# Performance work log

Hardware: AMD Instinct MI355X
Metric: run time of the kernel (lower is better)

The kernel has to match this reference:

```python
import jax, jax.numpy as jnp
import numpy as np

B, N, C, H, DEPTH, MLP = 8, 1024, 768, 12, 8, 3072
HD = C // H
SCALE = HD ** -0.5
EPS = 1e-5


def layer_norm(x, g, b):
    mu = jnp.mean(x, -1, keepdims=True)
    var = jnp.mean((x - mu) ** 2, -1, keepdims=True)
    return (x - mu) / jnp.sqrt(var + EPS) * g + b


def setup_inputs() -> dict:
    key = jax.random.key(0)
    ks = jax.random.split(key, 8)
    s = 0.02
    return {
        "x": jax.random.normal(ks[0], (B, N, C), jnp.float32),
        "ln1_g": jnp.ones((DEPTH, C), jnp.float32),
        "ln1_b": jnp.zeros((DEPTH, C), jnp.float32),
        "wqkv": jax.random.normal(ks[1], (DEPTH, C, 3 * C), jnp.float32) * s,
        "wproj": jax.random.normal(ks[2], (DEPTH, C, C), jnp.float32) * s,
        "bproj": jnp.zeros((DEPTH, C), jnp.float32),
        "ln2_g": jnp.ones((DEPTH, C), jnp.float32),
        "ln2_b": jnp.zeros((DEPTH, C), jnp.float32),
        "w1": jax.random.normal(ks[3], (DEPTH, C, MLP), jnp.float32) * s,
        "b1": jnp.zeros((DEPTH, MLP), jnp.float32),
        "w2": jax.random.normal(ks[4], (DEPTH, MLP, C), jnp.float32) * s,
        "b2": jnp.zeros((DEPTH, C), jnp.float32),
    }


def reference(x, ln1_g, ln1_b, wqkv, wproj, bproj, ln2_g, ln2_b, w1, b1, w2, b2):
    def body(h, p):
        g1, be1, wq, wp, bp, g2, be2, wf1, bf1, wf2, bf2 = p
        # --- attention block: Residual(PreNorm(SelfAttention)) ---
        y = layer_norm(h, g1, be1)
        qkv = (y @ wq).reshape(B, N, 3, H, HD)
        qkv = jnp.transpose(qkv, (2, 0, 3, 1, 4))  # [3, B, H, N, HD]
        q, k, v = qkv[0], qkv[1], qkv[2]
        logits = jnp.einsum("bhnd,bhmd->bhnm", q, k) * SCALE
        # source applies softmax twice (faithful to original)
        attn = jax.nn.softmax(jax.nn.softmax(logits, axis=-1), axis=-1)
        o = jnp.einsum("bhnm,bhmd->bhnd", attn, v)
        o = jnp.transpose(o, (0, 2, 1, 3)).reshape(B, N, C)
        h = h + o @ wp + bp
        # --- FFN block: Residual(PreNorm(FeedForward)) ---
        y2 = layer_norm(h, g2, be2)
        f = jax.nn.relu(y2 @ wf1 + bf1) @ wf2 + bf2
        return h + f, None

    out, _ = jax.lax.scan(body, x, (ln1_g, ln1_b, wqkv, wproj, bproj, ln2_g, ln2_b, w1, b1, w2, b2))
    return out
```

## Files before the change

kernel.cpp:

```cpp
#include <hip/hip_runtime.h>

#define DEPTHL 8
#define BZ 8
#define SEQ 1024
#define CDIM 768
#define HEADS 12
#define HDIM 64
#define MLPD 3072
#define TOK (BZ*SEQ)
#define QKVN (3*CDIM)

typedef __attribute__((ext_vector_type(8))) short vshort8;
typedef __attribute__((ext_vector_type(4))) short vshort4;
typedef __attribute__((ext_vector_type(4))) float vfloat4;

__device__ __forceinline__ short bf16_bits(float f) {
  union { float f; unsigned u; } x; x.f = f;
  unsigned r = (x.u + 0x7FFFu + ((x.u >> 16) & 1u)) >> 16;
  return (short)r;
}

#define GL16(g, l) __builtin_amdgcn_global_load_lds( \
    (const __attribute__((address_space(1))) unsigned int*)(g), \
    (__attribute__((address_space(3))) unsigned int*)(l), 16, 0, 0)

__global__ __launch_bounds__(256) void wconv_t(const float* __restrict__ in,
                                               short* __restrict__ out,
                                               int K, int N) {
  __shared__ float tile[32][33];
  const long d = blockIdx.z;
  in  += d * (long)K * N;
  out += d * (long)N * K;
  const int n0 = blockIdx.x * 32, k0 = blockIdx.y * 32;
  const int tx = threadIdx.x & 31, ty = threadIdx.x >> 5;
#pragma unroll
  for (int i = 0; i < 4; i++)
    tile[ty + 8*i][tx] = in[(long)(k0 + ty + 8*i) * N + n0 + tx];
  __syncthreads();
#pragma unroll
  for (int i = 0; i < 4; i++)
    out[(long)(n0 + ty + 8*i) * K + k0 + tx] = bf16_bits(tile[tx][ty + 8*i]);
}

__global__ __launch_bounds__(256) void vtrans(const short* __restrict__ qkv,
                                              short* __restrict__ vt) {
  __shared__ short tile[32][34];
  const int bh = blockIdx.z;
  const int b = bh / HEADS, hh = bh % HEADS;
  const int t0 = blockIdx.x * 32, d0 = blockIdx.y * 32;
  const int tx = threadIdx.x & 31, ty = threadIdx.x >> 5;
  const short* src = qkv + ((long)b * SEQ + t0) * QKVN + 2 * CDIM + hh * HDIM + d0;
#pragma unroll
  for (int i = 0; i < 4; i++)
    tile[ty + 8*i][tx] = src[(long)(ty + 8*i) * QKVN + tx];
  __syncthreads();
  short* dst = vt + (long)bh * HDIM * SEQ + (long)d0 * SEQ + t0;
#pragma unroll
  for (int i = 0; i < 4; i++)
    dst[(long)(ty + 8*i) * SEQ + tx] = tile[tx][ty + 8*i];
}

__global__ __launch_bounds__(192) void ln_fwd(const float* __restrict__ h,
                                              const float* __restrict__ g,
                                              const float* __restrict__ be,
                                              short* __restrict__ y) {
  __shared__ float red[3];
  const int row = blockIdx.x;
  const int tid = threadIdx.x;
  const float4 v = ((const float4*)(h + (long)row * CDIM))[tid];
  float s = v.x + v.y + v.z + v.w;
#pragma unroll
  for (int m = 32; m >= 1; m >>= 1) s += __shfl_xor(s, m);
  if ((tid & 63) == 0) red[tid >> 6] = s;
  __syncthreads();
  const float mu = (red[0] + red[1] + red[2]) * (1.0f / CDIM);
  float dx = v.x - mu, dy = v.y - mu, dz = v.z - mu, dw = v.w - mu;
  float q = dx*dx + dy*dy + dz*dz + dw*dw;
  __syncthreads();
#pragma unroll
  for (int m = 32; m >= 1; m >>= 1) q += __shfl_xor(q, m);
  if ((tid & 63) == 0) red[tid >> 6] = q;
  __syncthreads();
  const float rstd = rsqrtf((red[0] + red[1] + red[2]) * (1.0f / CDIM) + 1e-5f);
  const float4 g4 = ((const float4*)g)[tid];
  const float4 b4 = ((const float4*)be)[tid];
  vshort4 o;
  o[0] = bf16_bits(dx * rstd * g4.x + b4.x);
  o[1] = bf16_bits(dy * rstd * g4.y + b4.y);
  o[2] = bf16_bits(dz * rstd * g4.z + b4.z);
  o[3] = bf16_bits(dw * rstd * g4.w + b4.w);
  *(vshort4*)(y + (long)row * CDIM + tid * 4) = o;
}

template<int EPI>
__global__ __launch_bounds__(256) void gemm_bt(const short* __restrict__ A,
                                               const short* __restrict__ Bt,
                                               const float* __restrict__ bias,
                                               void* __restrict__ Cout,
                                               int M, int N, int K) {
  __shared__ short As[128 * 32];
  __shared__ short Bs[128 * 32];
  const int tid = threadIdx.x;
  const int wid = tid >> 6, lane = tid & 63;
  const int lg = lane >> 4, lr = lane & 15;
  const int wm = wid >> 1, wn = wid & 1;
  const long by = blockIdx.y;
  const long bx = blockIdx.x;

  vfloat4 acc[4][4];
#pragma unroll
  for (int i = 0; i < 4; i++)
#pragma unroll
    for (int j = 0; j < 4; j++) acc[i][j] = (vfloat4){0.f, 0.f, 0.f, 0.f};

  const int c = wid * 64 + lane;
  const short* Ag0 = A  + (by * 128 +      (c >> 2)) * (long)K + (c & 3) * 8;
  const short* Ag1 = A  + (by * 128 + 64 + (c >> 2)) * (long)K + (c & 3) * 8;
  const short* Bg0 = Bt + (bx * 128 +      (c >> 2)) * (long)K + (c & 3) * 8;
  const short* Bg1 = Bt + (bx * 128 + 64 + (c >> 2)) * (long)K + (c & 3) * 8;
  short* Al = As + c * 8;
  short* Bl = Bs + c * 8;

  for (int kk = 0; kk < K; kk += 32) {
    __syncthreads();
    GL16(Ag0 + kk, Al);
    GL16(Ag1 + kk, Al + 2048);
    GL16(Bg0 + kk, Bl);
    GL16(Bg1 + kk, Bl + 2048);
    __syncthreads();
    vshort8 a[4], b[4];
#pragma unroll
    for (int mt = 0; mt < 4; mt++)
      a[mt] = *(const vshort8*)(As + (wm * 64 + mt * 16 + lr) * 32 + lg * 8);
#pragma unroll
    for (int nt = 0; nt < 4; nt++)
      b[nt] = *(const vshort8*)(Bs + (wn * 64 + nt * 16 + lr) * 32 + lg * 8);
#pragma unroll
    for (int mt = 0; mt < 4; mt++)
#pragma unroll
      for (int nt = 0; nt < 4; nt++)
        acc[mt][nt] = __builtin_amdgcn_mfma_f32_16x16x32_bf16(a[mt], b[nt], acc[mt][nt], 0, 0, 0);
  }

  const long row0 = by * 128 + wm * 64;
  const long col0 = bx * 128 + wn * 64;
#pragma unroll
  for (int mt = 0; mt < 4; mt++) {
#pragma unroll
    for (int nt = 0; nt < 4; nt++) {
      const long col = col0 + nt * 16 + lr;
      float bv = 0.f;
      if (EPI != 0) bv = bias[col];
#pragma unroll
      for (int r = 0; r < 4; r++) {
        const long row = row0 + mt * 16 + lg * 4 + r;
        float v = acc[mt][nt][r];
        if (EPI == 0) {
          ((short*)Cout)[row * N + col] = bf16_bits(v);
        } else if (EPI == 1) {
          v += bv; v = v > 0.f ? v : 0.f;
          ((short*)Cout)[row * N + col] = bf16_bits(v);
        } else {
          float* hp = (float*)Cout + row * N + col;
          *hp = *hp + v + bv;
        }
      }
    }
  }
}

__global__ __launch_bounds__(256) void attn_fused2(const short* __restrict__ qkv,
                                                   const short* __restrict__ vt,
                                                   short* __restrict__ o) {
  __shared__ short P_lds[16 * 1024];
  __shared__ float redm[4][16], redz[4][16], redt[4][16];
  const int qt = blockIdx.x, bh = blockIdx.y;
  const int b = bh / HEADS, hh = bh % HEADS;
  const int tid = threadIdx.x, wid = tid >> 6, lane = tid & 63;
  const int lg = lane >> 4, lr = lane & 15;
  const long tokbase = (long)b * SEQ;
  const short* qbase = qkv + tokbase * QKVN + hh * HDIM;
  const short* kbase = qbase + CDIM;
  const short* vtb = vt + (long)bh * HDIM * SEQ;

  vshort8 qf[2];
#pragma unroll
  for (int ks = 0; ks < 2; ks++)
    qf[ks] = *(const vshort8*)(qbase + (long)(qt * 16 + lr) * QKVN + ks * 32 + lg * 8);

  vfloat4 s[16];
#pragma unroll
  for (int i = 0; i < 16; i++) {
    const int n0 = wid * 256 + i * 16;
    vfloat4 acc = (vfloat4){0.f, 0.f, 0.f, 0.f};
#pragma unroll
    for (int ks = 0; ks < 2; ks++) {
      vshort8 kf = *(const vshort8*)(kbase + (long)(n0 + lr) * QKVN + ks * 32 + lg * 8);
      acc = __builtin_amdgcn_mfma_f32_16x16x32_bf16(kf, qf[ks], acc, 0, 0, 0);
    }
    s[i][0] = acc[0] * 0.125f; s[i][1] = acc[1] * 0.125f;
    s[i][2] = acc[2] * 0.125f; s[i][3] = acc[3] * 0.125f;
  }

  vfloat4 mv = s[0];
#pragma unroll
  for (int i = 1; i < 16; i++) {
    mv[0] = fmaxf(mv[0], s[i][0]); mv[1] = fmaxf(mv[1], s[i][1]);
    mv[2] = fmaxf(mv[2], s[i][2]); mv[3] = fmaxf(mv[3], s[i][3]);
  }
  float m = fmaxf(fmaxf(mv[0], mv[1]), fmaxf(mv[2], mv[3]));
  m = fmaxf(m, __shfl_xor(m, 16));
  m = fmaxf(m, __shfl_xor(m, 32));
  if (lane < 16) redm[wid][lr] = m;
  __syncthreads();
  m = fmaxf(fmaxf(redm[0][lr], redm[1][lr]), fmaxf(redm[2][lr], redm[3][lr]));

  float z = 0.f;
#pragma unroll
  for (int i = 0; i < 16; i++) {
#pragma unroll
    for (int r = 0; r < 4; r++) { s[i][r] = __expf(s[i][r] - m); z += s[i][r]; }
  }
  z += __shfl_xor(z, 16);
  z += __shfl_xor(z, 32);
  if (lane < 16) redz[wid][lr] = z;
  __syncthreads();
  z = redz[0][lr] + redz[1][lr] + redz[2][lr] + redz[3][lr];
  const float rz = 1.0f / z;

  float t2 = 0.f;
#pragma unroll
  for (int i = 0; i < 16; i++) {
#pragma unroll
    for (int r = 0; r < 4; r++) { s[i][r] = __expf(s[i][r] * rz); t2 += s[i][r]; }
  }
  t2 += __shfl_xor(t2, 16);
  t2 += __shfl_xor(t2, 32);
  if (lane < 16) redt[wid][lr] = t2;
  __syncthreads();
  t2 = redt[0][lr] + redt[1][lr] + redt[2][lr] + redt[3][lr];
  const float rt = 1.0f / t2;

#pragma unroll
  for (int i = 0; i < 16; i++) {
    const int sbase = lr * 1024 + wid * 256 + i * 16 + lg * 4;
    const int byt = (sbase * 2) ^ ((lr & 7) << 4);
    vshort4 pk;
    pk[0] = bf16_bits(s[i][0] * rt); pk[1] = bf16_bits(s[i][1] * rt);
    pk[2] = bf16_bits(s[i][2] * rt); pk[3] = bf16_bits(s[i][3] * rt);
    *(vshort4*)((char*)P_lds + byt) = pk;
  }
  __syncthreads();

  const int dt = wid;
  vfloat4 oacc = (vfloat4){0.f, 0.f, 0.f, 0.f};
  const short* vrow = vtb + (long)(dt * 16 + lr) * SEQ + lg * 8;
#pragma unroll 8
  for (int win = 0; win < 32; win++) {
    const int abyt = (lr * 2048 + win * 64 + lg * 16) ^ ((lr & 7) << 4);
    vshort8 af = *(const vshort8*)((char*)P_lds + abyt);
    vshort8 bfr = *(const vshort8*)(vrow + win * 32);
    oacc = __builtin_amdgcn_mfma_f32_16x16x32_bf16(af, bfr, oacc, 0, 0, 0);
  }

#pragma unroll
  for (int r = 0; r < 4; r++) {
    const long row = tokbase + qt * 16 + lg * 4 + r;
    o[row * CDIM + hh * HDIM + dt * 16 + lr] = bf16_bits(oacc[r]);
  }
}

extern "C" void kernel_launch(void* const* d_in, const int* in_sizes, int n_in,
                              void* d_out, int out_size, void* d_ws, size_t ws_size,
                              hipStream_t stream) {
  const float* x     = (const float*)d_in[0];
  const float* ln1_g = (const float*)d_in[1];
  const float* ln1_b = (const float*)d_in[2];
  const float* wqkv  = (const float*)d_in[3];
  const float* wproj = (const float*)d_in[4];
  const float* bproj = (const float*)d_in[5];
  const float* ln2_g = (const float*)d_in[6];
  const float* ln2_b = (const float*)d_in[7];
  const float* w1    = (const float*)d_in[8];
  const float* b1    = (const float*)d_in[9];
  const float* w2    = (const float*)d_in[10];
  const float* b2    = (const float*)d_in[11];
  float* h = (float*)d_out;

  char* ws = (char*)d_ws;
  short* wqkv_t  = (short*)ws; ws += (size_t)DEPTHL * QKVN * CDIM * 2;
  short* wproj_t = (short*)ws; ws += (size_t)DEPTHL * CDIM * CDIM * 2;
  short* w1_t    = (short*)ws; ws += (size_t)DEPTHL * MLPD * CDIM * 2;
  short* w2_t    = (short*)ws; ws += (size_t)DEPTHL * CDIM * MLPD * 2;
  short* ybf     = (short*)ws; ws += (size_t)TOK * CDIM * 2;
  short* qkvbf   = (short*)ws; ws += (size_t)TOK * QKVN * 2;
  short* obf     = (short*)ws; ws += (size_t)TOK * CDIM * 2;
  short* f1bf    = (short*)ws; ws += (size_t)TOK * MLPD * 2;
  short* vtb     = f1bf;

  hipMemcpyAsync(h, x, (size_t)TOK * CDIM * sizeof(float), hipMemcpyDeviceToDevice, stream);

  wconv_t<<<dim3(QKVN / 32, CDIM / 32, DEPTHL), 256, 0, stream>>>(wqkv, wqkv_t, CDIM, QKVN);
  wconv_t<<<dim3(CDIM / 32, CDIM / 32, DEPTHL), 256, 0, stream>>>(wproj, wproj_t, CDIM, CDIM);
  wconv_t<<<dim3(MLPD / 32, CDIM / 32, DEPTHL), 256, 0, stream>>>(w1, w1_t, CDIM, MLPD);
  wconv_t<<<dim3(CDIM / 32, MLPD / 32, DEPTHL), 256, 0, stream>>>(w2, w2_t, MLPD, CDIM);

  for (int l = 0; l < DEPTHL; l++) {
    ln_fwd<<<TOK, 192, 0, stream>>>(h, ln1_g + l * CDIM, ln1_b + l * CDIM, ybf);
    gemm_bt<0><<<dim3(QKVN / 128, TOK / 128), 256, 0, stream>>>(
        ybf, wqkv_t + (size_t)l * QKVN * CDIM, nullptr, qkvbf, TOK, QKVN, CDIM);
    vtrans<<<dim3(SEQ / 32, HDIM / 32, BZ * HEADS), 256, 0, stream>>>(qkvbf, vtb);
    attn_fused2<<<dim3(SEQ / 16, BZ * HEADS), 256, 0, stream>>>(qkvbf, vtb, obf);
    gemm_bt<2><<<dim3(CDIM / 128, TOK / 128), 256, 0, stream>>>(
        obf, wproj_t + (size_t)l * CDIM * CDIM, bproj + l * CDIM, h, TOK, CDIM, CDIM);
    ln_fwd<<<TOK, 192, 0, stream>>>(h, ln2_g + l * CDIM, ln2_b + l * CDIM, ybf);
    gemm_bt<1><<<dim3(MLPD / 128, TOK / 128), 256, 0, stream>>>(
        ybf, w1_t + (size_t)l * MLPD * CDIM, b1 + l * MLPD, f1bf, TOK, MLPD, CDIM);
    gemm_bt<2><<<dim3(CDIM / 128, TOK / 128), 256, 0, stream>>>(
        f1bf, w2_t + (size_t)l * CDIM * MLPD, b2 + l * CDIM, h, TOK, CDIM, MLPD);
  }
}
```

Baseline: 3.589 ms.

## Remap workgroups XCD-aware and batch loads ahead of MFMAs in attention

Both the GEMM and the attention kernel now remap the flat workgroup id so consecutive logical tiles land on the same XCD (the id is strided by 8), which is meant to improve L2 reuse of shared A/B tiles and K/V rows. The attention kernel also batches the K-fragment and P/V loads into groups of four before issuing the MFMAs, so more memory requests are in flight, and it sets a launch-bounds occupancy hint of 2. The extra live registers could lower occupancy, and the remap assumes the grid size is divisible by 8.

```diff
diff --git a/kernel.cpp b/kernel.cpp
--- a/kernel.cpp
+++ b/kernel.cpp
@@ -104,8 +104,13 @@
   const int wid = tid >> 6, lane = tid & 63;
   const int lg = lane >> 4, lr = lane & 15;
   const int wm = wid >> 1, wn = wid & 1;
-  const long by = blockIdx.y;
-  const long bx = blockIdx.x;
+
+  const int gx = gridDim.x;
+  const int nwg = gx * gridDim.y;
+  int flat = blockIdx.y * gx + blockIdx.x;
+  flat = (flat & 7) * (nwg >> 3) + (flat >> 3);
+  const long bx = flat % gx;
+  const long by = flat / gx;
 
   vfloat4 acc[4][4];
 #pragma unroll
@@ -169,18 +174,21 @@
   }
 }
 
-__global__ __launch_bounds__(256) void attn_fused2(const short* __restrict__ qkv,
-                                                   const short* __restrict__ vt,
-                                                   short* __restrict__ o) {
+__global__ __launch_bounds__(256, 2) void attn_fused3(const short* __restrict__ qkv,
+                                                      const short* __restrict__ vt,
+                                                      short* __restrict__ o) {
   __shared__ short P_lds[16 * 1024];
   __shared__ float redm[4][16], redz[4][16], redt[4][16];
-  const int qt = blockIdx.x, bh = blockIdx.y;
+  int flat = blockIdx.y * 64 + blockIdx.x;
+  flat = (flat & 7) * (6144 >> 3) + (flat >> 3);
+  const int qt = flat & 63;
+  const int bh = flat >> 6;
   const int b = bh / HEADS, hh = bh % HEADS;
   const int tid = threadIdx.x, wid = tid >> 6, lane = tid & 63;
   const int lg = lane >> 4, lr = lane & 15;
   const long tokbase = (long)b * SEQ;
   const short* qbase = qkv + tokbase * QKVN + hh * HDIM;
-  const short* kbase = qbase + CDIM;
+  const short* kbase = qkv + tokbase * QKVN + CDIM + hh * HDIM;
   const short* vtb = vt + (long)bh * HDIM * SEQ;
 
   vshort8 qf[2];
@@ -190,16 +198,24 @@
 
   vfloat4 s[16];
 #pragma unroll
-  for (int i = 0; i < 16; i++) {
-    const int n0 = wid * 256 + i * 16;
-    vfloat4 acc = (vfloat4){0.f, 0.f, 0.f, 0.f};
-#pragma unroll
-    for (int ks = 0; ks < 2; ks++) {
-      vshort8 kf = *(const vshort8*)(kbase + (long)(n0 + lr) * QKVN + ks * 32 + lg * 8);
-      acc = __builtin_amdgcn_mfma_f32_16x16x32_bf16(kf, qf[ks], acc, 0, 0, 0);
+  for (int bb = 0; bb < 4; bb++) {
+    vshort8 kf[8];
+#pragma unroll
+    for (int u = 0; u < 4; u++) {
+      const int n0 = wid * 256 + (bb * 4 + u) * 16;
+#pragma unroll
+      for (int ks = 0; ks < 2; ks++)
+        kf[u * 2 + ks] = *(const vshort8*)(kbase + (long)(n0 + lr) * QKVN + ks * 32 + lg * 8);
     }
-    s[i][0] = acc[0] * 0.125f; s[i][1] = acc[1] * 0.125f;
-    s[i][2] = acc[2] * 0.125f; s[i][3] = acc[3] * 0.125f;
+#pragma unroll
+    for (int u = 0; u < 4; u++) {
+      vfloat4 acc = (vfloat4){0.f, 0.f, 0.f, 0.f};
+      acc = __builtin_amdgcn_mfma_f32_16x16x32_bf16(kf[u * 2 + 0], qf[0], acc, 0, 0, 0);
+      acc = __builtin_amdgcn_mfma_f32_16x16x32_bf16(kf[u * 2 + 1], qf[1], acc, 0, 0, 0);
+      const int i = bb * 4 + u;
+      s[i][0] = acc[0] * 0.125f; s[i][1] = acc[1] * 0.125f;
+      s[i][2] = acc[2] * 0.125f; s[i][3] = acc[3] * 0.125f;
+    }
   }
 
   vfloat4 mv = s[0];
@@ -255,12 +271,19 @@
   const int dt = wid;
   vfloat4 oacc = (vfloat4){0.f, 0.f, 0.f, 0.f};
   const short* vrow = vtb + (long)(dt * 16 + lr) * SEQ + lg * 8;
-#pragma unroll 8
-  for (int win = 0; win < 32; win++) {
-    const int abyt = (lr * 2048 + win * 64 + lg * 16) ^ ((lr & 7) << 4);
-    vshort8 af = *(const vshort8*)((char*)P_lds + abyt);
-    vshort8 bfr = *(const vshort8*)(vrow + win * 32);
-    oacc = __builtin_amdgcn_mfma_f32_16x16x32_bf16(af, bfr, oacc, 0, 0, 0);
+#pragma unroll
+  for (int bb = 0; bb < 8; bb++) {
+    vshort8 ab[4], vb[4];
+#pragma unroll
+    for (int u = 0; u < 4; u++) {
+      const int win = bb * 4 + u;
+      const int abyt = (lr * 2048 + win * 64 + lg * 16) ^ ((lr & 7) << 4);
+      ab[u] = *(const vshort8*)((char*)P_lds + abyt);
+      vb[u] = *(const vshort8*)(vrow + win * 32);
+    }
+#pragma unroll
+    for (int u = 0; u < 4; u++)
+      oacc = __builtin_amdgcn_mfma_f32_16x16x32_bf16(ab[u], vb[u], oacc, 0, 0, 0);
   }
 
 #pragma unroll
@@ -310,7 +333,7 @@
     gemm_bt<0><<<dim3(QKVN / 128, TOK / 128), 256, 0, stream>>>(
         ybf, wqkv_t + (size_t)l * QKVN * CDIM, nullptr, qkvbf, TOK, QKVN, CDIM);
     vtrans<<<dim3(SEQ / 32, HDIM / 32, BZ * HEADS), 256, 0, stream>>>(qkvbf, vtb);
-    attn_fused2<<<dim3(SEQ / 16, BZ * HEADS), 256, 0, stream>>>(qkvbf, vtb, obf);
+    attn_fused3<<<dim3(SEQ / 16, BZ * HEADS), 256, 0, stream>>>(qkvbf, vtb, obf);
     gemm_bt<2><<<dim3(CDIM / 128, TOK / 128), 256, 0, stream>>>(
         obf, wproj_t + (size_t)l * CDIM * CDIM, bproj + l * CDIM, h, TOK, CDIM, CDIM);
     ln_fwd<<<TOK, 192, 0, stream>>>(h, ln2_g + l * CDIM, ln2_b + l * CDIM, ybf);
```

After: 3.510 ms. -2.2%, faster.
